# Kernel optimization log

Measured on AMD Instinct MI355X. Metric: run time of the kernel, lower is better.

## Reference

```python
import jax, jax.numpy as jnp
import numpy as np
from jax import lax

B, T, X, Y = 32, 64, 64, 64
DT = 0.2        # T_points[1] - T_points[0]
DX = 1.0        # X_points[1] - X_points[0]
EPS = 1.0
C = DT / DX**2  # explicit-Euler stencil coefficient (0.2 < 0.25, stable)


def laplace_2d(u):
    # u: [B, X, Y]. Interior: 5-point second differences; edges (not corners)
    # patched with periodic BC; corners stay at their partial-interior value (0).
    out = jnp.zeros_like(u)
    out = out.at[:, 1:-1, :].add(jnp.diff(jnp.diff(u, axis=1), axis=1))
    out = out.at[:, :, 1:-1].add(jnp.diff(jnp.diff(u, axis=2), axis=2))
    out = out.at[:, 0, 1:-1].set(u[:, 1, 1:-1] + u[:, -1, 1:-1] + u[:, 0, :-2] + u[:, 0, 2:] - 4 * u[:, 0, 1:-1])
    out = out.at[:, -1, 1:-1].set(u[:, 0, 1:-1] + u[:, -2, 1:-1] + u[:, -1, :-2] + u[:, -1, 2:] - 4 * u[:, -1, 1:-1])
    out = out.at[:, 1:-1, 0].set(u[:, 1:-1, 1] + u[:, 1:-1, -1] + u[:, :-2, 0] + u[:, 2:, 0] - 4 * u[:, 1:-1, 0])
    out = out.at[:, 1:-1, -1].set(u[:, 1:-1, 0] + u[:, 1:-1, -2] + u[:, :-2, -1] + u[:, 2:, -1] - 4 * u[:, 1:-1, -1])
    return out * C


def integrate(f):
    # f: [B, T, X, Y] forcing. res[0]=0; res[i] = res[i-1] + eps*L(res[i-1]) + f[i-1]*dt
    u0 = jnp.zeros(f.shape[:1] + f.shape[2:], f.dtype)  # [B, X, Y]
    fs = jnp.moveaxis(f[:, :-1], 1, 0)  # [T-1, B, X, Y]

    def step(u, ft):
        u = u + EPS * laplace_2d(u) + ft * DT
        return u, u

    _, us = lax.scan(step, u0, fs)
    return jnp.concatenate([u0[:, None], jnp.moveaxis(us, 0, 1)], axis=1)  # [B, T, X, Y]


def discrete_diff_2d(v, axis):
    # Faithful to torch discrete_diff_2d with higher=False on a 4D [B,T,X,Y] tensor:
    # axis=1 operates on dim 1 (T), axis=2 on dim 2 (X), exactly as the slicing does.
    a = jnp.zeros_like(v)
    if axis == 1:
        body = -jnp.roll(v[:, :-1, :, :], 1, axis=1)
        a = a.at[:, :-1].set(body)
        a = a.at[:, -1].set(body[:, 0])
    else:
        body = -jnp.roll(v[:, :, :-1, :], 1, axis=2)
        a = a.at[:, :, :-1].set(body)
        a = a.at[:, :, -1].set(body[:, :, 0])
    return a


def setup_inputs() -> dict:
    key = jax.random.key(0)
    W = jax.random.normal(key, (B, T, X, Y), dtype=jnp.float32)
    return {"W": W}


def reference(W):
    # node 0: xi -> dW = time-diff of W / dt (first slice zeros)
    dW = jnp.zeros_like(W).at[:, 1:].set(jnp.diff(W, axis=1) / DT)
    # node 1: I[xi]
    I_xi = integrate(dW)
    # nodes 2,3: derivatives of I[xi]
    I1 = discrete_diff_2d(I_xi, 1) / DX
    I2 = discrete_diff_2d(I_xi, 2) / DX
    # node 4: I[xi * I[xi]]
    f4 = integrate(dW * I_xi)
    # node 5: I[I[xi]^2]
    f5 = integrate(I_xi ** 2)
    # node 6: I[I1[I[xi]] * I2[I[xi]]]
    f6 = integrate(I1 * I2)
    return jnp.stack([dW, I_xi, I1, I2, f4, f5, f6], axis=-1)  # [B,T,X,Y,7]
```

## Files before the change

### kernel.cpp

```cpp
#include <hip/hip_runtime.h>

namespace {

constexpr float C2  = 0.2f;
constexpr float DTC = 0.2f;
constexpr float IDT = 5.0f;

__device__ __forceinline__ int ldsOff(int row, int q) {
    return ((row << 4) + (q ^ (row & 15))) << 2;
}

__global__ __launch_bounds__(512, 2)
void fused_scan(const float* __restrict__ W, float* __restrict__ out) {
    __shared__ float sxi[2][4096];
    __shared__ float s4 [2][4096];
    __shared__ float s5 [2][4096];
    __shared__ float s6 [2][4096];

    const int tid  = threadIdx.x;
    const int b    = blockIdx.x >> 3;
    const int part = blockIdx.x & 7;

    const int x   = tid >> 3;
    const int ycc = tid & 7;
    const int yo  = ycc << 3;
    const int q0  = ycc << 1;

    const bool mine = ((tid >> 6) == part);

    const int lane   = tid & 63;
    const int laneYm = (lane & 56) | ((ycc - 1) & 7);
    const int laneYp = (lane & 56) | ((ycc + 1) & 7);

    const int xm = (x + 63) & 63;
    const int xp = (x + 1) & 63;

    const bool xedge = (x == 0) || (x == 63);
    const bool crn0  = xedge && (ycc == 0);
    const bool crn7  = xedge && (ycc == 7);

    float cxi[8], c4[8], c5[8], c6[8], xprev[8], wprev[8];
    #pragma unroll
    for (int j = 0; j < 8; ++j) {
        cxi[j] = 0.0f; c4[j] = 0.0f; c5[j] = 0.0f; c6[j] = 0.0f;
        xprev[j] = 0.0f; wprev[j] = 0.0f;
    }

    const float4 z4 = make_float4(0.0f, 0.0f, 0.0f, 0.0f);
    #pragma unroll
    for (int h = 0; h < 2; ++h) {
        *(float4*)&sxi[0][ldsOff(x, q0 + h)] = z4;
        *(float4*)&s4 [0][ldsOff(x, q0 + h)] = z4;
        *(float4*)&s5 [0][ldsOff(x, q0 + h)] = z4;
        *(float4*)&s6 [0][ldsOff(x, q0 + h)] = z4;
    }
    __syncthreads();

    const float* Wb = W   + (size_t)b * 64 * 4096;
    float*       oB = out + (size_t)b * 64 * 4096 * 7;

    float wt[8];
    {
        const float* wp = Wb + x * 64 + yo;
        *(float4*)&wt[0] = *(const float4*)(wp);
        *(float4*)&wt[4] = *(const float4*)(wp + 4);
    }

    int cb = 0;
    for (int t = 0; t < 64; ++t) {
        float wnext[8];
        if (t < 63) {
            const float* wp = Wb + (t + 1) * 4096 + x * 64 + yo;
            *(float4*)&wnext[0] = *(const float4*)(wp);
            *(float4*)&wnext[4] = *(const float4*)(wp + 4);
        }

        float dw[8];
        #pragma unroll
        for (int j = 0; j < 8; ++j)
            dw[j] = (t == 0) ? 0.0f : (wt[j] - wprev[j]) * IDT;
        #pragma unroll
        for (int j = 0; j < 8; ++j) wprev[j] = wt[j];

        float nbm[8], nbp[8];
        *(float4*)&nbm[0] = *(const float4*)&sxi[cb][ldsOff(xm, q0)];
        *(float4*)&nbm[4] = *(const float4*)&sxi[cb][ldsOff(xm, q0 + 1)];
        *(float4*)&nbp[0] = *(const float4*)&sxi[cb][ldsOff(xp, q0)];
        *(float4*)&nbp[4] = *(const float4*)&sxi[cb][ldsOff(xp, q0 + 1)];

        float xi2[8];
        if (x == 0) {
            *(float4*)&xi2[0] = *(const float4*)&sxi[cb][ldsOff(62, q0)];
            *(float4*)&xi2[4] = *(const float4*)&sxi[cb][ldsOff(62, q0 + 1)];
        } else {
            #pragma unroll
            for (int j = 0; j < 8; ++j) xi2[j] = nbm[j];
        }

        if (mine) {
            #pragma unroll
            for (int h = 0; h < 2; ++h) {
                float4 ov[7];
                float* o = (float*)ov;
                #pragma unroll
                for (int j = 0; j < 4; ++j) {
                    const int jj = (h << 2) + j;
                    o[j * 7 + 0] = dw[jj];
                    o[j * 7 + 1] = cxi[jj];
                    o[j * 7 + 2] = (t == 0) ? 0.0f : -xprev[jj];
                    o[j * 7 + 3] = -xi2[jj];
                    o[j * 7 + 4] = c4[jj];
                    o[j * 7 + 5] = c5[jj];
                    o[j * 7 + 6] = c6[jj];
                }
                float4* dst = (float4*)(oB + ((size_t)t * 4096 + x * 64 + yo + (h << 2)) * 7);
                #pragma unroll
                for (int k = 0; k < 7; ++k) dst[k] = ov[k];
            }
        }

        if (t == 63) {
            if (mine) {
                float* p0 = oB + (size_t)(x * 64 + yo) * 7 + 2;
                #pragma unroll
                for (int j = 0; j < 8; ++j) p0[j * 7] = -xprev[j];
            }
        } else {
            const int nb = cb ^ 1;

            float g4v[8], g5v[8], g6v[8];
            #pragma unroll
            for (int j = 0; j < 8; ++j) {
                g4v[j] = dw[j] * cxi[j];
                g5v[j] = cxi[j] * cxi[j];
                g6v[j] = xprev[j] * xi2[j];
            }
            #pragma unroll
            for (int j = 0; j < 8; ++j) xprev[j] = cxi[j];

            auto stepCore = [&](float* c, const float* nm, const float* np_,
                                const float* g) {
                const float ym = __shfl(c[7], laneYm, 64);
                const float yp = __shfl(c[0], laneYp, 64);
                float n[8];
                #pragma unroll
                for (int j = 0; j < 8; ++j) {
                    const float left  = (j == 0) ? ym : c[j - 1];
                    const float right = (j == 7) ? yp : c[j + 1];
                    float lap = nm[j] + np_[j] + left + right - 4.0f * c[j];
                    if ((j == 0 && crn0) || (j == 7 && crn7)) lap = 0.0f;
                    n[j] = c[j] + C2 * lap + g[j] * DTC;
                }
                #pragma unroll
                for (int j = 0; j < 8; ++j) c[j] = n[j];
            };
            auto stepField = [&](const float* sArr, float* c, const float* g) {
                float nm[8], np_[8];
                *(float4*)&nm[0]  = *(const float4*)&sArr[ldsOff(xm, q0)];
                *(float4*)&nm[4]  = *(const float4*)&sArr[ldsOff(xm, q0 + 1)];
                *(float4*)&np_[0] = *(const float4*)&sArr[ldsOff(xp, q0)];
                *(float4*)&np_[4] = *(const float4*)&sArr[ldsOff(xp, q0 + 1)];
                stepCore(c, nm, np_, g);
            };

            stepCore (cxi, nbm, nbp, dw);
            stepField(&s4[cb][0], c4, g4v);
            stepField(&s5[cb][0], c5, g5v);
            stepField(&s6[cb][0], c6, g6v);

            #pragma unroll
            for (int h = 0; h < 2; ++h) {
                *(float4*)&sxi[nb][ldsOff(x, q0 + h)] = *(float4*)&cxi[h << 2];
                *(float4*)&s4 [nb][ldsOff(x, q0 + h)] = *(float4*)&c4 [h << 2];
                *(float4*)&s5 [nb][ldsOff(x, q0 + h)] = *(float4*)&c5 [h << 2];
                *(float4*)&s6 [nb][ldsOff(x, q0 + h)] = *(float4*)&c6 [h << 2];
            }
            __syncthreads();
            cb = nb;
        }

        #pragma unroll
        for (int j = 0; j < 8; ++j) wt[j] = wnext[j];
    }
}

}

extern "C" void kernel_launch(void* const* d_in, const int* in_sizes, int n_in,
                              void* d_out, int out_size, void* d_ws, size_t ws_size,
                              hipStream_t stream) {
    const float* W  = (const float*)d_in[0];
    float* out      = (float*)d_out;
    hipLaunchKernelGGL(fused_scan, dim3(256), dim3(512), 0, stream, W, out);
}
```

Before: 342.3 us.

## Use 1024-thread blocks with 4 y-points per thread

Doubles the block size to 1024 threads so each thread owns 4 consecutive y-points instead of 8, halving per-thread register state and LDS traffic per step. Output ownership is now split into 8 parts of 128 threads, and block-to-batch mapping is interleaved (b = blockIdx & 31) so that concurrently scheduled blocks cover different batches. The aim is more latency hiding per CU for the serial time scan. The cost is heavier barrier synchronization across 16 waves and the same redundant recomputation of the full grid in each of the 8 blocks per batch.

```diff
diff --git a/kernel.cpp b/kernel.cpp
--- a/kernel.cpp
+++ b/kernel.cpp
@@ -10,7 +10,7 @@
     return ((row << 4) + (q ^ (row & 15))) << 2;
 }
 
-__global__ __launch_bounds__(512, 2)
+__global__ __launch_bounds__(1024, 4)
 void fused_scan(const float* __restrict__ W, float* __restrict__ out) {
     __shared__ float sxi[2][4096];
     __shared__ float s4 [2][4096];
@@ -18,148 +18,129 @@
     __shared__ float s6 [2][4096];
 
     const int tid  = threadIdx.x;
-    const int b    = blockIdx.x >> 3;
-    const int part = blockIdx.x & 7;
+    const int b    = blockIdx.x & 31;
+    const int part = blockIdx.x >> 5;
 
-    const int x   = tid >> 3;
-    const int ycc = tid & 7;
-    const int yo  = ycc << 3;
-    const int q0  = ycc << 1;
+    const int x  = tid >> 4;
+    const int yc = tid & 15;
+    const int yo = yc << 2;
+    const int q0 = yc;
 
-    const bool mine = ((tid >> 6) == part);
+    const bool mine = ((tid >> 7) == part);
 
     const int lane   = tid & 63;
-    const int laneYm = (lane & 56) | ((ycc - 1) & 7);
-    const int laneYp = (lane & 56) | ((ycc + 1) & 7);
+    const int laneYm = (lane & 48) | ((yc - 1) & 15);
+    const int laneYp = (lane & 48) | ((yc + 1) & 15);
 
     const int xm = (x + 63) & 63;
     const int xp = (x + 1) & 63;
 
     const bool xedge = (x == 0) || (x == 63);
-    const bool crn0  = xedge && (ycc == 0);
-    const bool crn7  = xedge && (ycc == 7);
+    const bool crnLo = xedge && (yc == 0);
+    const bool crnHi = xedge && (yc == 15);
 
-    float cxi[8], c4[8], c5[8], c6[8], xprev[8], wprev[8];
+    float cxi[4], c4[4], c5[4], c6[4], xprev[4], wprev[4];
     #pragma unroll
-    for (int j = 0; j < 8; ++j) {
+    for (int j = 0; j < 4; ++j) {
         cxi[j] = 0.0f; c4[j] = 0.0f; c5[j] = 0.0f; c6[j] = 0.0f;
         xprev[j] = 0.0f; wprev[j] = 0.0f;
     }
 
     const float4 z4 = make_float4(0.0f, 0.0f, 0.0f, 0.0f);
-    #pragma unroll
-    for (int h = 0; h < 2; ++h) {
-        *(float4*)&sxi[0][ldsOff(x, q0 + h)] = z4;
-        *(float4*)&s4 [0][ldsOff(x, q0 + h)] = z4;
-        *(float4*)&s5 [0][ldsOff(x, q0 + h)] = z4;
-        *(float4*)&s6 [0][ldsOff(x, q0 + h)] = z4;
-    }
+    *(float4*)&sxi[0][ldsOff(x, q0)] = z4;
+    *(float4*)&s4 [0][ldsOff(x, q0)] = z4;
+    *(float4*)&s5 [0][ldsOff(x, q0)] = z4;
+    *(float4*)&s6 [0][ldsOff(x, q0)] = z4;
     __syncthreads();
 
     const float* Wb = W   + (size_t)b * 64 * 4096;
     float*       oB = out + (size_t)b * 64 * 4096 * 7;
 
-    float wt[8];
-    {
-        const float* wp = Wb + x * 64 + yo;
-        *(float4*)&wt[0] = *(const float4*)(wp);
-        *(float4*)&wt[4] = *(const float4*)(wp + 4);
-    }
+    float wt[4];
+    *(float4*)&wt[0] = *(const float4*)(Wb + x * 64 + yo);
 
     int cb = 0;
     for (int t = 0; t < 64; ++t) {
-        float wnext[8];
-        if (t < 63) {
-            const float* wp = Wb + (t + 1) * 4096 + x * 64 + yo;
-            *(float4*)&wnext[0] = *(const float4*)(wp);
-            *(float4*)&wnext[4] = *(const float4*)(wp + 4);
-        }
+        float wnext[4];
+        if (t < 63)
+            *(float4*)&wnext[0] = *(const float4*)(Wb + (t + 1) * 4096 + x * 64 + yo);
 
-        float dw[8];
+        float dw[4];
         #pragma unroll
-        for (int j = 0; j < 8; ++j)
+        for (int j = 0; j < 4; ++j)
             dw[j] = (t == 0) ? 0.0f : (wt[j] - wprev[j]) * IDT;
         #pragma unroll
-        for (int j = 0; j < 8; ++j) wprev[j] = wt[j];
+        for (int j = 0; j < 4; ++j) wprev[j] = wt[j];
 
-        float nbm[8], nbp[8];
+        float nbm[4], nbp[4];
         *(float4*)&nbm[0] = *(const float4*)&sxi[cb][ldsOff(xm, q0)];
-        *(float4*)&nbm[4] = *(const float4*)&sxi[cb][ldsOff(xm, q0 + 1)];
         *(float4*)&nbp[0] = *(const float4*)&sxi[cb][ldsOff(xp, q0)];
-        *(float4*)&nbp[4] = *(const float4*)&sxi[cb][ldsOff(xp, q0 + 1)];
 
-        float xi2[8];
+        float xi2[4];
         if (x == 0) {
             *(float4*)&xi2[0] = *(const float4*)&sxi[cb][ldsOff(62, q0)];
-            *(float4*)&xi2[4] = *(const float4*)&sxi[cb][ldsOff(62, q0 + 1)];
         } else {
             #pragma unroll
-            for (int j = 0; j < 8; ++j) xi2[j] = nbm[j];
+            for (int j = 0; j < 4; ++j) xi2[j] = nbm[j];
         }
 
         if (mine) {
+            float4 ov[7];
+            float* o = (float*)ov;
             #pragma unroll
-            for (int h = 0; h < 2; ++h) {
-                float4 ov[7];
-                float* o = (float*)ov;
-                #pragma unroll
-                for (int j = 0; j < 4; ++j) {
-                    const int jj = (h << 2) + j;
-                    o[j * 7 + 0] = dw[jj];
-                    o[j * 7 + 1] = cxi[jj];
-                    o[j * 7 + 2] = (t == 0) ? 0.0f : -xprev[jj];
-                    o[j * 7 + 3] = -xi2[jj];
-                    o[j * 7 + 4] = c4[jj];
-                    o[j * 7 + 5] = c5[jj];
-                    o[j * 7 + 6] = c6[jj];
-                }
-                float4* dst = (float4*)(oB + ((size_t)t * 4096 + x * 64 + yo + (h << 2)) * 7);
-                #pragma unroll
-                for (int k = 0; k < 7; ++k) dst[k] = ov[k];
+            for (int j = 0; j < 4; ++j) {
+                o[j * 7 + 0] = dw[j];
+                o[j * 7 + 1] = cxi[j];
+                o[j * 7 + 2] = (t == 0) ? 0.0f : -xprev[j];
+                o[j * 7 + 3] = -xi2[j];
+                o[j * 7 + 4] = c4[j];
+                o[j * 7 + 5] = c5[j];
+                o[j * 7 + 6] = c6[j];
             }
+            float4* dst = (float4*)(oB + ((size_t)t * 4096 + x * 64 + yo) * 7);
+            #pragma unroll
+            for (int k = 0; k < 7; ++k) dst[k] = ov[k];
         }
 
         if (t == 63) {
             if (mine) {
                 float* p0 = oB + (size_t)(x * 64 + yo) * 7 + 2;
                 #pragma unroll
-                for (int j = 0; j < 8; ++j) p0[j * 7] = -xprev[j];
+                for (int j = 0; j < 4; ++j) p0[j * 7] = -xprev[j];
             }
         } else {
             const int nb = cb ^ 1;
 
-            float g4v[8], g5v[8], g6v[8];
+            float g4v[4], g5v[4], g6v[4];
             #pragma unroll
-            for (int j = 0; j < 8; ++j) {
+            for (int j = 0; j < 4; ++j) {
                 g4v[j] = dw[j] * cxi[j];
                 g5v[j] = cxi[j] * cxi[j];
                 g6v[j] = xprev[j] * xi2[j];
             }
             #pragma unroll
-            for (int j = 0; j < 8; ++j) xprev[j] = cxi[j];
+            for (int j = 0; j < 4; ++j) xprev[j] = cxi[j];
 
             auto stepCore = [&](float* c, const float* nm, const float* np_,
                                 const float* g) {
-                const float ym = __shfl(c[7], laneYm, 64);
+                const float ym = __shfl(c[3], laneYm, 64);
                 const float yp = __shfl(c[0], laneYp, 64);
-                float n[8];
+                float n[4];
                 #pragma unroll
-                for (int j = 0; j < 8; ++j) {
+                for (int j = 0; j < 4; ++j) {
                     const float left  = (j == 0) ? ym : c[j - 1];
-                    const float right = (j == 7) ? yp : c[j + 1];
+                    const float right = (j == 3) ? yp : c[j + 1];
                     float lap = nm[j] + np_[j] + left + right - 4.0f * c[j];
-                    if ((j == 0 && crn0) || (j == 7 && crn7)) lap = 0.0f;
+                    if ((j == 0 && crnLo) || (j == 3 && crnHi)) lap = 0.0f;
                     n[j] = c[j] + C2 * lap + g[j] * DTC;
                 }
                 #pragma unroll
-                for (int j = 0; j < 8; ++j) c[j] = n[j];
+                for (int j = 0; j < 4; ++j) c[j] = n[j];
             };
             auto stepField = [&](const float* sArr, float* c, const float* g) {
-                float nm[8], np_[8];
+                float nm[4], np_[4];
                 *(float4*)&nm[0]  = *(const float4*)&sArr[ldsOff(xm, q0)];
-                *(float4*)&nm[4]  = *(const float4*)&sArr[ldsOff(xm, q0 + 1)];
                 *(float4*)&np_[0] = *(const float4*)&sArr[ldsOff(xp, q0)];
-                *(float4*)&np_[4] = *(const float4*)&sArr[ldsOff(xp, q0 + 1)];
                 stepCore(c, nm, np_, g);
             };
 
@@ -168,19 +149,16 @@
             stepField(&s5[cb][0], c5, g5v);
             stepField(&s6[cb][0], c6, g6v);
 
-            #pragma unroll
-            for (int h = 0; h < 2; ++h) {
-                *(float4*)&sxi[nb][ldsOff(x, q0 + h)] = *(float4*)&cxi[h << 2];
-                *(float4*)&s4 [nb][ldsOff(x, q0 + h)] = *(float4*)&c4 [h << 2];
-                *(float4*)&s5 [nb][ldsOff(x, q0 + h)] = *(float4*)&c5 [h << 2];
-                *(float4*)&s6 [nb][ldsOff(x, q0 + h)] = *(float4*)&c6 [h << 2];
-            }
+            *(float4*)&sxi[nb][ldsOff(x, q0)] = *(float4*)&cxi[0];
+            *(float4*)&s4 [nb][ldsOff(x, q0)] = *(float4*)&c4 [0];
+            *(float4*)&s5 [nb][ldsOff(x, q0)] = *(float4*)&c5 [0];
+            *(float4*)&s6 [nb][ldsOff(x, q0)] = *(float4*)&c6 [0];
             __syncthreads();
             cb = nb;
+
+            #pragma unroll
+            for (int j = 0; j < 4; ++j) wt[j] = wnext[j];
         }
-
-        #pragma unroll
-        for (int j = 0; j < 8; ++j) wt[j] = wnext[j];
     }
 }
 
@@ -191,5 +169,5 @@
                               hipStream_t stream) {
     const float* W  = (const float*)d_in[0];
     float* out      = (float*)d_out;
-    hipLaunchKernelGGL(fused_scan, dim3(256), dim3(512), 0, stream, W, out);
+    hipLaunchKernelGGL(fused_scan, dim3(256), dim3(1024), 0, stream, W, out);
 }
```

Result: slower. 360.3 us (+5.3%).

## Split auxiliary scan fields across blocks instead of computing all redundantly

Applied to the files above, without the earlier changes.

Each block now advances the xi field plus only one of the three auxiliary integrals, chosen by a group index, and writes half of the x rows. Before, every block carried all four fields and wrote one eighth of the rows. This removes redundant stencil work and halves LDS per block, which may allow more concurrent blocks. In exchange, output stores become scalar stride-7 writes to interleaved channels, so different blocks write to the same cache lines and coalescing is worse than the previous float4 stores.

```diff
diff --git a/kernel.cpp b/kernel.cpp
--- a/kernel.cpp
+++ b/kernel.cpp
@@ -6,27 +6,26 @@
 constexpr float DTC = 0.2f;
 constexpr float IDT = 5.0f;
 
-__device__ __forceinline__ int ldsOff(int row, int q) {
-    return ((row << 4) + (q ^ (row & 15))) << 2;
+__device__ __forceinline__ int ldsOff(int row, int ycc, int h) {
+    return ((row << 4) + ((ycc + (h << 3)) ^ (row & 15))) << 2;
 }
 
 __global__ __launch_bounds__(512, 2)
 void fused_scan(const float* __restrict__ W, float* __restrict__ out) {
     __shared__ float sxi[2][4096];
-    __shared__ float s4 [2][4096];
-    __shared__ float s5 [2][4096];
-    __shared__ float s6 [2][4096];
+    __shared__ float sex[2][4096];
 
-    const int tid  = threadIdx.x;
-    const int b    = blockIdx.x >> 3;
-    const int part = blockIdx.x & 7;
+    const int tid   = threadIdx.x;
+    const int b     = blockIdx.x & 31;
+    const int gi    = blockIdx.x >> 5;
+    const int group = gi >> 1;
+    const int part  = gi & 1;
 
     const int x   = tid >> 3;
     const int ycc = tid & 7;
     const int yo  = ycc << 3;
-    const int q0  = ycc << 1;
 
-    const bool mine = ((tid >> 6) == part);
+    const bool mine = ((x >> 5) == part);
 
     const int lane   = tid & 63;
     const int laneYm = (lane & 56) | ((ycc - 1) & 7);
@@ -39,20 +38,17 @@
     const bool crn0  = xedge && (ycc == 0);
     const bool crn7  = xedge && (ycc == 7);
 
-    float cxi[8], c4[8], c5[8], c6[8], xprev[8], wprev[8];
+    float cxi[8], cex[8], xprev[8], wprev[8];
     #pragma unroll
     for (int j = 0; j < 8; ++j) {
-        cxi[j] = 0.0f; c4[j] = 0.0f; c5[j] = 0.0f; c6[j] = 0.0f;
-        xprev[j] = 0.0f; wprev[j] = 0.0f;
+        cxi[j] = 0.0f; cex[j] = 0.0f; xprev[j] = 0.0f; wprev[j] = 0.0f;
     }
 
     const float4 z4 = make_float4(0.0f, 0.0f, 0.0f, 0.0f);
     #pragma unroll
     for (int h = 0; h < 2; ++h) {
-        *(float4*)&sxi[0][ldsOff(x, q0 + h)] = z4;
-        *(float4*)&s4 [0][ldsOff(x, q0 + h)] = z4;
-        *(float4*)&s5 [0][ldsOff(x, q0 + h)] = z4;
-        *(float4*)&s6 [0][ldsOff(x, q0 + h)] = z4;
+        *(float4*)&sxi[0][ldsOff(x, ycc, h)] = z4;
+        *(float4*)&sex[0][ldsOff(x, ycc, h)] = z4;
     }
     __syncthreads();
 
@@ -83,44 +79,40 @@
         for (int j = 0; j < 8; ++j) wprev[j] = wt[j];
 
         float nbm[8], nbp[8];
-        *(float4*)&nbm[0] = *(const float4*)&sxi[cb][ldsOff(xm, q0)];
-        *(float4*)&nbm[4] = *(const float4*)&sxi[cb][ldsOff(xm, q0 + 1)];
-        *(float4*)&nbp[0] = *(const float4*)&sxi[cb][ldsOff(xp, q0)];
-        *(float4*)&nbp[4] = *(const float4*)&sxi[cb][ldsOff(xp, q0 + 1)];
+        *(float4*)&nbm[0] = *(const float4*)&sxi[cb][ldsOff(xm, ycc, 0)];
+        *(float4*)&nbm[4] = *(const float4*)&sxi[cb][ldsOff(xm, ycc, 1)];
+        *(float4*)&nbp[0] = *(const float4*)&sxi[cb][ldsOff(xp, ycc, 0)];
+        *(float4*)&nbp[4] = *(const float4*)&sxi[cb][ldsOff(xp, ycc, 1)];
 
         float xi2[8];
         if (x == 0) {
-            *(float4*)&xi2[0] = *(const float4*)&sxi[cb][ldsOff(62, q0)];
-            *(float4*)&xi2[4] = *(const float4*)&sxi[cb][ldsOff(62, q0 + 1)];
+            *(float4*)&xi2[0] = *(const float4*)&sxi[cb][ldsOff(62, ycc, 0)];
+            *(float4*)&xi2[4] = *(const float4*)&sxi[cb][ldsOff(62, ycc, 1)];
         } else {
             #pragma unroll
             for (int j = 0; j < 8; ++j) xi2[j] = nbm[j];
         }
 
         if (mine) {
-            #pragma unroll
-            for (int h = 0; h < 2; ++h) {
-                float4 ov[7];
-                float* o = (float*)ov;
+            float* base = oB + ((size_t)t * 4096 + x * 64 + yo) * 7;
+            if (group == 0) {
                 #pragma unroll
-                for (int j = 0; j < 4; ++j) {
-                    const int jj = (h << 2) + j;
-                    o[j * 7 + 0] = dw[jj];
-                    o[j * 7 + 1] = cxi[jj];
-                    o[j * 7 + 2] = (t == 0) ? 0.0f : -xprev[jj];
-                    o[j * 7 + 3] = -xi2[jj];
-                    o[j * 7 + 4] = c4[jj];
-                    o[j * 7 + 5] = c5[jj];
-                    o[j * 7 + 6] = c6[jj];
+                for (int j = 0; j < 8; ++j) {
+                    base[j * 7 + 0] = dw[j];
+                    base[j * 7 + 1] = cxi[j];
+                    base[j * 7 + 2] = (t == 0) ? 0.0f : -xprev[j];
+                    base[j * 7 + 3] = -xi2[j];
                 }
-                float4* dst = (float4*)(oB + ((size_t)t * 4096 + x * 64 + yo + (h << 2)) * 7);
+            } else {
+                const int ch = group + 3;
                 #pragma unroll
-                for (int k = 0; k < 7; ++k) dst[k] = ov[k];
+                for (int j = 0; j < 8; ++j)
+                    base[j * 7 + ch] = cex[j];
             }
         }
 
         if (t == 63) {
-            if (mine) {
+            if (mine && group == 0) {
                 float* p0 = oB + (size_t)(x * 64 + yo) * 7 + 2;
                 #pragma unroll
                 for (int j = 0; j < 8; ++j) p0[j * 7] = -xprev[j];
@@ -128,12 +120,16 @@
         } else {
             const int nb = cb ^ 1;
 
-            float g4v[8], g5v[8], g6v[8];
-            #pragma unroll
-            for (int j = 0; j < 8; ++j) {
-                g4v[j] = dw[j] * cxi[j];
-                g5v[j] = cxi[j] * cxi[j];
-                g6v[j] = xprev[j] * xi2[j];
+            float ge[8];
+            if (group <= 1) {
+                #pragma unroll
+                for (int j = 0; j < 8; ++j) ge[j] = dw[j] * cxi[j];
+            } else if (group == 2) {
+                #pragma unroll
+                for (int j = 0; j < 8; ++j) ge[j] = cxi[j] * cxi[j];
+            } else {
+                #pragma unroll
+                for (int j = 0; j < 8; ++j) ge[j] = xprev[j] * xi2[j];
             }
             #pragma unroll
             for (int j = 0; j < 8; ++j) xprev[j] = cxi[j];
@@ -154,33 +150,29 @@
                 #pragma unroll
                 for (int j = 0; j < 8; ++j) c[j] = n[j];
             };
-            auto stepField = [&](const float* sArr, float* c, const float* g) {
+
+            stepCore(cxi, nbm, nbp, dw);
+
+            {
                 float nm[8], np_[8];
-                *(float4*)&nm[0]  = *(const float4*)&sArr[ldsOff(xm, q0)];
-                *(float4*)&nm[4]  = *(const float4*)&sArr[ldsOff(xm, q0 + 1)];
-                *(float4*)&np_[0] = *(const float4*)&sArr[ldsOff(xp, q0)];
-                *(float4*)&np_[4] = *(const float4*)&sArr[ldsOff(xp, q0 + 1)];
-                stepCore(c, nm, np_, g);
-            };
-
-            stepCore (cxi, nbm, nbp, dw);
-            stepField(&s4[cb][0], c4, g4v);
-            stepField(&s5[cb][0], c5, g5v);
-            stepField(&s6[cb][0], c6, g6v);
+                *(float4*)&nm[0]  = *(const float4*)&sex[cb][ldsOff(xm, ycc, 0)];
+                *(float4*)&nm[4]  = *(const float4*)&sex[cb][ldsOff(xm, ycc, 1)];
+                *(float4*)&np_[0] = *(const float4*)&sex[cb][ldsOff(xp, ycc, 0)];
+                *(float4*)&np_[4] = *(const float4*)&sex[cb][ldsOff(xp, ycc, 1)];
+                stepCore(cex, nm, np_, ge);
+            }
 
             #pragma unroll
             for (int h = 0; h < 2; ++h) {
-                *(float4*)&sxi[nb][ldsOff(x, q0 + h)] = *(float4*)&cxi[h << 2];
-                *(float4*)&s4 [nb][ldsOff(x, q0 + h)] = *(float4*)&c4 [h << 2];
-                *(float4*)&s5 [nb][ldsOff(x, q0 + h)] = *(float4*)&c5 [h << 2];
-                *(float4*)&s6 [nb][ldsOff(x, q0 + h)] = *(float4*)&c6 [h << 2];
+                *(float4*)&sxi[nb][ldsOff(x, ycc, h)] = *(float4*)&cxi[h << 2];
+                *(float4*)&sex[nb][ldsOff(x, ycc, h)] = *(float4*)&cex[h << 2];
             }
             __syncthreads();
             cb = nb;
+
+            #pragma unroll
+            for (int j = 0; j < 8; ++j) wt[j] = wnext[j];
         }
-
-        #pragma unroll
-        for (int j = 0; j < 8; ++j) wt[j] = wnext[j];
     }
 }
 
```

Result: slower. 410.1 us (+19.8%).

## Replace block barriers with neighbor-wave LDS flags and rotate output-writing wave

Applied to the files above, without the earlier changes.

Each wave now waits only on its two ring neighbours, using per-wave write/read progress counters in LDS, instead of a full __syncthreads each time step. This lets waves drift apart and overlap compute with global stores. The wave that writes output rotates with t so store work is spread across waves. Block-to-batch mapping is changed, all neighbour LDS loads are hoisted ahead of the output stores, and waves start staggered with s_sleep. The risks are spin-wait overhead and subtle memory-ordering errors, since the flag stores are relaxed and rely on explicit lgkmcnt waits.

```diff
diff --git a/kernel.cpp b/kernel.cpp
--- a/kernel.cpp
+++ b/kernel.cpp
@@ -6,8 +6,8 @@
 constexpr float DTC = 0.2f;
 constexpr float IDT = 5.0f;
 
-__device__ __forceinline__ int ldsOff(int row, int q) {
-    return ((row << 4) + (q ^ (row & 15))) << 2;
+__device__ __forceinline__ int ldsOff(int row, int ycc, int h) {
+    return ((row << 4) + ((ycc + (h << 3)) ^ (row & 15))) << 2;
 }
 
 __global__ __launch_bounds__(512, 2)
@@ -16,17 +16,19 @@
     __shared__ float s4 [2][4096];
     __shared__ float s5 [2][4096];
     __shared__ float s6 [2][4096];
+    __shared__ int   wdone[8];
+    __shared__ int   rdone[8];
 
     const int tid  = threadIdx.x;
-    const int b    = blockIdx.x >> 3;
-    const int part = blockIdx.x & 7;
+    const int b    = blockIdx.x & 31;
+    const int part = blockIdx.x >> 5;
 
     const int x   = tid >> 3;
     const int ycc = tid & 7;
     const int yo  = ycc << 3;
-    const int q0  = ycc << 1;
-
-    const bool mine = ((tid >> 6) == part);
+    const int wv  = tid >> 6;
+    const int wm1 = (wv + 7) & 7;
+    const int wp1 = (wv + 1) & 7;
 
     const int lane   = tid & 63;
     const int laneYm = (lane & 56) | ((ycc - 1) & 7);
@@ -46,15 +48,21 @@
         xprev[j] = 0.0f; wprev[j] = 0.0f;
     }
 
+    if (tid < 8) {
+        __hip_atomic_store(&wdone[tid], 0,  __ATOMIC_RELAXED, __HIP_MEMORY_SCOPE_WORKGROUP);
+        __hip_atomic_store(&rdone[tid], -1, __ATOMIC_RELAXED, __HIP_MEMORY_SCOPE_WORKGROUP);
+    }
     const float4 z4 = make_float4(0.0f, 0.0f, 0.0f, 0.0f);
     #pragma unroll
     for (int h = 0; h < 2; ++h) {
-        *(float4*)&sxi[0][ldsOff(x, q0 + h)] = z4;
-        *(float4*)&s4 [0][ldsOff(x, q0 + h)] = z4;
-        *(float4*)&s5 [0][ldsOff(x, q0 + h)] = z4;
-        *(float4*)&s6 [0][ldsOff(x, q0 + h)] = z4;
+        *(float4*)&sxi[0][ldsOff(x, ycc, h)] = z4;
+        *(float4*)&s4 [0][ldsOff(x, ycc, h)] = z4;
+        *(float4*)&s5 [0][ldsOff(x, ycc, h)] = z4;
+        *(float4*)&s6 [0][ldsOff(x, ycc, h)] = z4;
     }
     __syncthreads();
+
+    for (int i = 0; i < wv; ++i) __builtin_amdgcn_s_sleep(2);
 
     const float* Wb = W   + (size_t)b * 64 * 4096;
     float*       oB = out + (size_t)b * 64 * 4096 * 7;
@@ -82,22 +90,42 @@
         #pragma unroll
         for (int j = 0; j < 8; ++j) wprev[j] = wt[j];
 
+        while (__hip_atomic_load(&wdone[wm1], __ATOMIC_ACQUIRE, __HIP_MEMORY_SCOPE_WORKGROUP) < t) {}
+        while (__hip_atomic_load(&wdone[wp1], __ATOMIC_ACQUIRE, __HIP_MEMORY_SCOPE_WORKGROUP) < t) {}
+
         float nbm[8], nbp[8];
-        *(float4*)&nbm[0] = *(const float4*)&sxi[cb][ldsOff(xm, q0)];
-        *(float4*)&nbm[4] = *(const float4*)&sxi[cb][ldsOff(xm, q0 + 1)];
-        *(float4*)&nbp[0] = *(const float4*)&sxi[cb][ldsOff(xp, q0)];
-        *(float4*)&nbp[4] = *(const float4*)&sxi[cb][ldsOff(xp, q0 + 1)];
+        *(float4*)&nbm[0] = *(const float4*)&sxi[cb][ldsOff(xm, ycc, 0)];
+        *(float4*)&nbm[4] = *(const float4*)&sxi[cb][ldsOff(xm, ycc, 1)];
+        *(float4*)&nbp[0] = *(const float4*)&sxi[cb][ldsOff(xp, ycc, 0)];
+        *(float4*)&nbp[4] = *(const float4*)&sxi[cb][ldsOff(xp, ycc, 1)];
 
         float xi2[8];
         if (x == 0) {
-            *(float4*)&xi2[0] = *(const float4*)&sxi[cb][ldsOff(62, q0)];
-            *(float4*)&xi2[4] = *(const float4*)&sxi[cb][ldsOff(62, q0 + 1)];
+            *(float4*)&xi2[0] = *(const float4*)&sxi[cb][ldsOff(62, ycc, 0)];
+            *(float4*)&xi2[4] = *(const float4*)&sxi[cb][ldsOff(62, ycc, 1)];
         } else {
             #pragma unroll
             for (int j = 0; j < 8; ++j) xi2[j] = nbm[j];
         }
 
-        if (mine) {
+        float nm4[8], np4[8], nm5[8], np5[8], nm6[8], np6[8];
+        *(float4*)&nm4[0] = *(const float4*)&s4[cb][ldsOff(xm, ycc, 0)];
+        *(float4*)&nm4[4] = *(const float4*)&s4[cb][ldsOff(xm, ycc, 1)];
+        *(float4*)&np4[0] = *(const float4*)&s4[cb][ldsOff(xp, ycc, 0)];
+        *(float4*)&np4[4] = *(const float4*)&s4[cb][ldsOff(xp, ycc, 1)];
+        *(float4*)&nm5[0] = *(const float4*)&s5[cb][ldsOff(xm, ycc, 0)];
+        *(float4*)&nm5[4] = *(const float4*)&s5[cb][ldsOff(xm, ycc, 1)];
+        *(float4*)&np5[0] = *(const float4*)&s5[cb][ldsOff(xp, ycc, 0)];
+        *(float4*)&np5[4] = *(const float4*)&s5[cb][ldsOff(xp, ycc, 1)];
+        *(float4*)&nm6[0] = *(const float4*)&s6[cb][ldsOff(xm, ycc, 0)];
+        *(float4*)&nm6[4] = *(const float4*)&s6[cb][ldsOff(xm, ycc, 1)];
+        *(float4*)&np6[0] = *(const float4*)&s6[cb][ldsOff(xp, ycc, 0)];
+        *(float4*)&np6[4] = *(const float4*)&s6[cb][ldsOff(xp, ycc, 1)];
+
+        asm volatile("s_waitcnt lgkmcnt(0)" ::: "memory");
+        __hip_atomic_store(&rdone[wv], t, __ATOMIC_RELAXED, __HIP_MEMORY_SCOPE_WORKGROUP);
+
+        if (wv == ((part + t) & 7)) {
             #pragma unroll
             for (int h = 0; h < 2; ++h) {
                 float4 ov[7];
@@ -119,15 +147,7 @@
             }
         }
 
-        if (t == 63) {
-            if (mine) {
-                float* p0 = oB + (size_t)(x * 64 + yo) * 7 + 2;
-                #pragma unroll
-                for (int j = 0; j < 8; ++j) p0[j * 7] = -xprev[j];
-            }
-        } else {
-            const int nb = cb ^ 1;
-
+        if (t < 63) {
             float g4v[8], g5v[8], g6v[8];
             #pragma unroll
             for (int j = 0; j < 8; ++j) {
@@ -154,33 +174,36 @@
                 #pragma unroll
                 for (int j = 0; j < 8; ++j) c[j] = n[j];
             };
-            auto stepField = [&](const float* sArr, float* c, const float* g) {
-                float nm[8], np_[8];
-                *(float4*)&nm[0]  = *(const float4*)&sArr[ldsOff(xm, q0)];
-                *(float4*)&nm[4]  = *(const float4*)&sArr[ldsOff(xm, q0 + 1)];
-                *(float4*)&np_[0] = *(const float4*)&sArr[ldsOff(xp, q0)];
-                *(float4*)&np_[4] = *(const float4*)&sArr[ldsOff(xp, q0 + 1)];
-                stepCore(c, nm, np_, g);
-            };
-
-            stepCore (cxi, nbm, nbp, dw);
-            stepField(&s4[cb][0], c4, g4v);
-            stepField(&s5[cb][0], c5, g5v);
-            stepField(&s6[cb][0], c6, g6v);
-
+
+            stepCore(cxi, nbm, nbp, dw);
+            stepCore(c4,  nm4, np4, g4v);
+            stepCore(c5,  nm5, np5, g5v);
+            stepCore(c6,  nm6, np6, g6v);
+
+            while (__hip_atomic_load(&rdone[wm1], __ATOMIC_ACQUIRE, __HIP_MEMORY_SCOPE_WORKGROUP) < t - 1) {}
+            while (__hip_atomic_load(&rdone[wp1], __ATOMIC_ACQUIRE, __HIP_MEMORY_SCOPE_WORKGROUP) < t - 1) {}
+
+            const int nb = cb ^ 1;
             #pragma unroll
             for (int h = 0; h < 2; ++h) {
-                *(float4*)&sxi[nb][ldsOff(x, q0 + h)] = *(float4*)&cxi[h << 2];
-                *(float4*)&s4 [nb][ldsOff(x, q0 + h)] = *(float4*)&c4 [h << 2];
-                *(float4*)&s5 [nb][ldsOff(x, q0 + h)] = *(float4*)&c5 [h << 2];
-                *(float4*)&s6 [nb][ldsOff(x, q0 + h)] = *(float4*)&c6 [h << 2];
+                *(float4*)&sxi[nb][ldsOff(x, ycc, h)] = *(float4*)&cxi[h << 2];
+                *(float4*)&s4 [nb][ldsOff(x, ycc, h)] = *(float4*)&c4 [h << 2];
+                *(float4*)&s5 [nb][ldsOff(x, ycc, h)] = *(float4*)&c5 [h << 2];
+                *(float4*)&s6 [nb][ldsOff(x, ycc, h)] = *(float4*)&c6 [h << 2];
             }
-            __syncthreads();
+            asm volatile("s_waitcnt lgkmcnt(0)" ::: "memory");
+            __hip_atomic_store(&wdone[wv], t + 1, __ATOMIC_RELAXED, __HIP_MEMORY_SCOPE_WORKGROUP);
             cb = nb;
-        }
-
+
+            #pragma unroll
+            for (int j = 0; j < 8; ++j) wt[j] = wnext[j];
+        }
+    }
+
+    if (wv == part) {
+        float* p0 = oB + (size_t)(x * 64 + yo) * 7 + 2;
         #pragma unroll
-        for (int j = 0; j < 8; ++j) wt[j] = wnext[j];
+        for (int j = 0; j < 8; ++j) p0[j * 7] = -xprev[j];
     }
 }
 
```

New measurement: 349.2 us. +2.0%, slower.
